# Performance work log

Hardware: AMD Instinct MI355X
Metric: run time of the kernel (lower is better)

The kernel has to match this reference:

```python
import jax, jax.numpy as jnp
import numpy as np

# Model config (matches init_kwargs)
HIDDEN = 2048
N_HEADS = 32
N_KV_HEADS = 8
HEAD_DIM = 64
BS = 8  # block_size_x = block_size_y = block_size_z


def setup_inputs() -> dict:
    key = jax.random.key(0)
    ks = jax.random.split(key, 5)
    B, X, Y, Z = 2, 16, 16, 16
    L = X * Y * Z  # 4096
    s = 1.0 / np.sqrt(HIDDEN)
    return {
        "hidden_states": jax.random.normal(ks[0], (B, L, HIDDEN), jnp.float32),
        "Wq": jax.random.normal(ks[1], (N_HEADS * HEAD_DIM, HIDDEN), jnp.float32) * s,
        "Wk": jax.random.normal(ks[2], (N_KV_HEADS * HEAD_DIM, HIDDEN), jnp.float32) * s,
        "Wv": jax.random.normal(ks[3], (N_KV_HEADS * HEAD_DIM, HIDDEN), jnp.float32) * s,
        "Wo": jax.random.normal(ks[4], (HIDDEN, N_HEADS * HEAD_DIM), jnp.float32) * s,
        "x_dim": 16,
        "y_dim": 16,
        "z_dim": 16,
    }


def _to_blocks(t, B, x_dim, y_dim, z_dim, H):
    # t: [B, L, H*D] with L interpreted as (x, y, z) row-major grid.
    # einops: 'b (bnx bsx bny bsy bnz bsz) (h d) -> (b bnx bny bnz) (bsx bsy bsz) h d'
    bnx, bny, bnz = x_dim // BS, y_dim // BS, z_dim // BS
    t = t.reshape(B, bnx, BS, bny, BS, bnz, BS, H, HEAD_DIM)
    t = t.transpose(0, 1, 3, 5, 2, 4, 6, 7, 8)  # [B,bnx,bny,bnz,bsx,bsy,bsz,H,D]
    return t.reshape(B * bnx * bny * bnz, BS * BS * BS, H, HEAD_DIM)


def _from_blocks(o, B, x_dim, y_dim, z_dim):
    bnx, bny, bnz = x_dim // BS, y_dim // BS, z_dim // BS
    o = o.reshape(B, bnx, bny, bnz, BS, BS, BS, N_HEADS, HEAD_DIM)
    o = o.transpose(0, 1, 4, 2, 5, 3, 6, 7, 8)  # back to (bnx bsx bny bsy bnz bsz)
    return o.reshape(B, x_dim * y_dim * z_dim, N_HEADS * HEAD_DIM)


def reference(hidden_states, Wq, Wk, Wv, Wo, x_dim, y_dim, z_dim):
    B, L, _ = hidden_states.shape
    q = _to_blocks(hidden_states @ Wq.T, B, x_dim, y_dim, z_dim, N_HEADS)     # [NB,T,H,D]
    k = _to_blocks(hidden_states @ Wk.T, B, x_dim, y_dim, z_dim, N_KV_HEADS)  # [NB,T,Hk,D]
    v = _to_blocks(hidden_states @ Wv.T, B, x_dim, y_dim, z_dim, N_KV_HEADS)
    # GQA: repeat kv heads across groups (flash_attn handles this internally)
    g = N_HEADS // N_KV_HEADS
    k = jnp.repeat(k, g, axis=2)
    v = jnp.repeat(v, g, axis=2)
    scale = HEAD_DIM ** -0.5
    # non-causal full attention within each 3D block
    scores = jnp.einsum('bthd,bshd->bhts', q, k) * scale  # [NB,H,T,T]
    p = jax.nn.softmax(scores, axis=-1)
    o = jnp.einsum('bhts,bshd->bthd', p, v)               # [NB,T,H,D]
    o = _from_blocks(o, B, x_dim, y_dim, z_dim)           # [B,L,H*D]
    return o @ Wo.T
```

## Files before the change

kernel.cpp:

```cpp
#include <hip/hip_runtime.h>

typedef _Float16 f16;
typedef _Float16 f16x4 __attribute__((ext_vector_type(4)));
typedef _Float16 f16x8 __attribute__((ext_vector_type(8)));
typedef float f32x4 __attribute__((ext_vector_type(4)));
typedef unsigned int u32;
typedef u32 u32x4 __attribute__((ext_vector_type(4)));

__device__ __forceinline__ f32x4 mfma16(f16x8 a, f16x8 b, f32x4 c) {
  return __builtin_amdgcn_mfma_f32_16x16x32_f16(a, b, c, 0, 0, 0);
}

__device__ __forceinline__ void gld_lds16(const void* g, void* l) {
  __builtin_amdgcn_global_load_lds(
      (const __attribute__((address_space(1))) void*)g,
      (__attribute__((address_space(3))) void*)l, 16, 0, 0);
}

__device__ __forceinline__ u32 pkrtz(float a, float b) {
  return __builtin_bit_cast(u32, __builtin_amdgcn_cvt_pkrtz(a, b));
}

#define XSWZ(row) (((row) & 7) << 4)

__global__ __launch_bounds__(256) void cast5_k(
    const float4* s0, const float4* s1, const float4* s2, const float4* s3,
    const float4* s4, f16x4* d0, f16x4* d1, f16x4* d2, f16x4* d3, f16x4* d4,
    int e0, int e1, int e2, int e3, int e4) {
  int i = blockIdx.x * blockDim.x + threadIdx.x;
  int stride = gridDim.x * blockDim.x;
  for (; i < e4; i += stride) {
    const float4* s = s0; f16x4* d = d0; int base = 0;
    if (i >= e0) { s = s1; d = d1; base = e0; }
    if (i >= e1) { s = s2; d = d2; base = e1; }
    if (i >= e2) { s = s3; d = d3; base = e2; }
    if (i >= e3) { s = s4; d = d4; base = e3; }
    float4 v = s[i - base];
    f16x4 o;
    o.x = (f16)v.x; o.y = (f16)v.y; o.z = (f16)v.z; o.w = (f16)v.w;
    d[i - base] = o;
  }
}

template <typename OutT>
__global__ __launch_bounds__(256, 2) void gemm_bt(
    const f16* __restrict__ A, const f16* __restrict__ B, OutT* __restrict__ C,
    int M, int N, int K, float oscale) {
  __shared__ __align__(16) f16 Al[128 * 64];
  __shared__ __align__(16) f16 Bl[128 * 64];
  const int tid = threadIdx.x;
  const int lane = tid & 63;
  const int wave = tid >> 6;
  const int bm = blockIdx.x, bn = blockIdx.y;
  const int wm = wave >> 1, wn = wave & 1;
  f32x4 acc[4][4] = {};

  const size_t ldb = (size_t)K * 2;
  const char* Ab = (const char*)A + (size_t)bm * 128 * ldb;
  const char* Bb = (const char*)B + (size_t)bn * 128 * ldb;

  const int kTiles = K >> 6;
  for (int kt = 0; kt < kTiles; ++kt) {
    const size_t kOff = (size_t)kt << 7;
    __syncthreads();
#pragma unroll
    for (int i = 0; i < 4; ++i) {
      int c = i * 256 + tid;
      int row = c >> 3;
      int colb = ((c & 7) << 4) ^ XSWZ(row);
      gld_lds16(Ab + (size_t)row * ldb + kOff + colb,
                (char*)Al + (i * 256 + wave * 64) * 16);
      gld_lds16(Bb + (size_t)row * ldb + kOff + colb,
                (char*)Bl + (i * 256 + wave * 64) * 16);
    }
    __syncthreads();
#pragma unroll
    for (int kk = 0; kk < 2; ++kk) {
      const int kb = kk * 64 + ((lane >> 4) << 4);
      f16x8 af[4], bf[4];
#pragma unroll
      for (int mf = 0; mf < 4; ++mf) {
        int row = wm * 64 + mf * 16 + (lane & 15);
        af[mf] = *(const f16x8*)((const char*)Al + (row << 7) + (kb ^ XSWZ(row)));
      }
#pragma unroll
      for (int nf = 0; nf < 4; ++nf) {
        int row = wn * 64 + nf * 16 + (lane & 15);
        bf[nf] = *(const f16x8*)((const char*)Bl + (row << 7) + (kb ^ XSWZ(row)));
      }
#pragma unroll
      for (int mf = 0; mf < 4; ++mf)
#pragma unroll
        for (int nf = 0; nf < 4; ++nf)
          acc[mf][nf] = mfma16(af[mf], bf[nf], acc[mf][nf]);
    }
  }
  const int r0 = ((lane >> 4) << 2);
  const int cl = lane & 15;
#pragma unroll
  for (int mf = 0; mf < 4; ++mf)
#pragma unroll
    for (int r = 0; r < 4; ++r) {
      size_t row = (size_t)bm * 128 + wm * 64 + mf * 16 + r0 + r;
#pragma unroll
      for (int nf = 0; nf < 4; ++nf) {
        int col = bn * 128 + wn * 64 + nf * 16 + cl;
        C[row * N + col] = (OutT)(acc[mf][nf][r] * oscale);
      }
    }
}

template <typename OutT>
__global__ __launch_bounds__(512, 2) void gemm_bt8(
    const f16* __restrict__ A, const f16* __restrict__ B, OutT* __restrict__ C,
    int M, int N, int K, float oscale) {
  __shared__ __align__(16) char lds[131072];
  const int tid = threadIdx.x;
  const int lane = tid & 63;
  const int wave = tid >> 6;
  const int wm = wave >> 2, wn = wave & 3;
  const int l15 = lane & 15, g = lane >> 4;
  const int bid = blockIdx.x;
  const int bm = (bid & 7) * 4 + ((bid >> 3) & 3);
  const int bn = bid >> 5;

  const size_t ldb = (size_t)K * 2;
  const int r0 = tid >> 2, r1 = 128 + (tid >> 2);
  const int chx = (((tid & 3) ^ ((tid >> 3) & 3)) << 4);
  const char* As0 = (const char*)A + (size_t)(bm * 256 + r0) * ldb + chx;
  const char* As1 = (const char*)A + (size_t)(bm * 256 + r1) * ldb + chx;
  const char* Bs0 = (const char*)B + (size_t)(bn * 256 + r0) * ldb + chx;
  const char* Bs1 = (const char*)B + (size_t)(bn * 256 + r1) * ldb + chx;

  auto stA = [&](int buf, int t, int kh) {
    char* dst = (char*)lds + (buf * 2 + kh) * 16384 + wave * 1024;
    size_t ko = (size_t)t * 128 + (size_t)kh * 64;
    gld_lds16(As0 + ko, dst);
    gld_lds16(As1 + ko, dst + 8192);
  };
  auto stB = [&](int buf, int t, int kh) {
    char* dst = (char*)lds + 65536 + (buf * 2 + kh) * 16384 + wave * 1024;
    size_t ko = (size_t)t * 128 + (size_t)kh * 64;
    gld_lds16(Bs0 + ko, dst);
    gld_lds16(Bs1 + ko, dst + 8192);
  };

  int aoff[8], boff[4];
  const int rsw = (g ^ ((l15 >> 1) & 3)) << 4;
#pragma unroll
  for (int mf = 0; mf < 8; ++mf)
    aoff[mf] = (wm * 128 + mf * 16 + l15) * 64 + rsw;
#pragma unroll
  for (int nf = 0; nf < 4; ++nf)
    boff[nf] = (wn * 64 + nf * 16 + l15) * 64 + rsw;

  f32x4 acc[8][4] = {};

  stA(0, 0, 0); stB(0, 0, 0); stA(0, 0, 1); stB(0, 0, 1);
  stA(1, 1, 0); stB(1, 1, 0); stA(1, 1, 1);
  asm volatile("s_waitcnt vmcnt(6)" ::: "memory");
  __builtin_amdgcn_s_barrier();

  const int nkt = K >> 6;
  for (int T = 0; T < nkt; ++T) {
    const int cur = T & 1;
    const char* A0 = (const char*)lds + (cur * 2 + 0) * 16384;
    const char* A1 = (const char*)lds + (cur * 2 + 1) * 16384;
    const char* B0r = (const char*)lds + 65536 + (cur * 2 + 0) * 16384;
    const char* B1r = (const char*)lds + 65536 + (cur * 2 + 1) * 16384;
    f16x8 a[8], b0, b1;
#pragma unroll
    for (int mf = 0; mf < 8; ++mf) a[mf] = *(const f16x8*)(A0 + aoff[mf]);
    b0 = *(const f16x8*)(B0r + boff[0]);
    b1 = *(const f16x8*)(B0r + boff[1]);
    if (T + 1 < nkt) stB(cur ^ 1, T + 1, 1);
    __builtin_amdgcn_s_barrier();
    __builtin_amdgcn_s_setprio(1);
#pragma unroll
    for (int mf = 0; mf < 8; ++mf) {
      acc[mf][0] = mfma16(a[mf], b0, acc[mf][0]);
      acc[mf][1] = mfma16(a[mf], b1, acc[mf][1]);
    }
    __builtin_amdgcn_s_setprio(0);
    __builtin_amdgcn_s_barrier();
    b0 = *(const f16x8*)(B0r + boff[2]);
    b1 = *(const f16x8*)(B0r + boff[3]);
    if (T + 2 < nkt) stA(cur, T + 2, 0);
    __builtin_amdgcn_s_barrier();
    __builtin_amdgcn_s_setprio(1);
#pragma unroll
    for (int mf = 0; mf < 8; ++mf) {
      acc[mf][2] = mfma16(a[mf], b0, acc[mf][2]);
      acc[mf][3] = mfma16(a[mf], b1, acc[mf][3]);
    }
    __builtin_amdgcn_s_setprio(0);
    __builtin_amdgcn_s_barrier();
#pragma unroll
    for (int mf = 0; mf < 8; ++mf) a[mf] = *(const f16x8*)(A1 + aoff[mf]);
    b0 = *(const f16x8*)(B1r + boff[0]);
    b1 = *(const f16x8*)(B1r + boff[1]);
    if (T + 2 < nkt) stB(cur, T + 2, 0);
    __builtin_amdgcn_s_barrier();
    __builtin_amdgcn_s_setprio(1);
#pragma unroll
    for (int mf = 0; mf < 8; ++mf) {
      acc[mf][0] = mfma16(a[mf], b0, acc[mf][0]);
      acc[mf][1] = mfma16(a[mf], b1, acc[mf][1]);
    }
    __builtin_amdgcn_s_setprio(0);
    __builtin_amdgcn_s_barrier();
    b0 = *(const f16x8*)(B1r + boff[2]);
    b1 = *(const f16x8*)(B1r + boff[3]);
    if (T + 2 < nkt) stA(cur, T + 2, 1);
    if (T < nkt - 2) asm volatile("s_waitcnt vmcnt(6)" ::: "memory");
    else             asm volatile("s_waitcnt vmcnt(0)" ::: "memory");
    __builtin_amdgcn_s_barrier();
    __builtin_amdgcn_s_setprio(1);
#pragma unroll
    for (int mf = 0; mf < 8; ++mf) {
      acc[mf][2] = mfma16(a[mf], b0, acc[mf][2]);
      acc[mf][3] = mfma16(a[mf], b1, acc[mf][3]);
    }
    __builtin_amdgcn_s_setprio(0);
    __builtin_amdgcn_s_barrier();
  }
#pragma unroll
  for (int mf = 0; mf < 8; ++mf)
#pragma unroll
    for (int r = 0; r < 4; ++r) {
      size_t row = (size_t)bm * 256 + wm * 128 + mf * 16 + g * 4 + r;
#pragma unroll
      for (int nf = 0; nf < 4; ++nf) {
        int col = bn * 256 + wn * 64 + nf * 16 + l15;
        C[row * (size_t)N + col] = (OutT)(acc[mf][nf][r] * oscale);
      }
    }
}

__device__ __forceinline__ int tok_row(int nb, int t) {
  int b = nb >> 3;
  int x = (((nb >> 2) & 1) << 3) | (t >> 6);
  int y = (((nb >> 1) & 1) << 3) | ((t >> 3) & 7);
  int z = ((nb & 1) << 3) | (t & 7);
  return (b << 12) | (x << 8) | (y << 4) | z;
}

__global__ __launch_bounds__(512) void attn3d(
    const f16* __restrict__ Q, const f16* __restrict__ KV, f16* __restrict__ O) {
  __shared__ __align__(16) f16 Ql[512 * 64];
  __shared__ __align__(16) f16 Kl[64 * 64];
  __shared__ __align__(16) f16 Vt[64 * 64];
  const int tid = threadIdx.x;
  const int lane = tid & 63;
  const int wave = tid >> 6;
  const int fid = blockIdx.x;
  const int orig = (fid & 7) * 64 + (fid >> 3);
  const int h = orig & 31, nb = orig >> 5;
  const int hk = h >> 2;
  const int l15 = lane & 15;
  const int g = lane >> 4;
  const size_t ldkv = 2048;

  const int pos2 = (((lane & 3) | (((lane >> 4) & 1) << 2) |
                     (((lane >> 2) & 3) << 3) | ((lane >> 5) << 5))) * 2;

#pragma unroll
  for (int i = 0; i < 8; ++i) {
    int c = i * 512 + tid;
    int row = c >> 3;
    int colb = ((c & 7) << 4) ^ XSWZ(row);
    gld_lds16((const char*)Q + (size_t)tok_row(nb, row) * 4096 + h * 128 + colb,
              (char*)Ql + (i * 512 + wave * 64) * 16);
  }
  __syncthreads();
  f16x8 bq[4][2];
#pragma unroll
  for (int qf = 0; qf < 4; ++qf)
#pragma unroll
    for (int kk = 0; kk < 2; ++kk) {
      int row = wave * 64 + qf * 16 + l15;
      int kb = kk * 64 + (g << 4);
      bq[qf][kk] = *(const f16x8*)((const char*)Ql + (row << 7) + (kb ^ XSWZ(row)));
    }

  f32x4 o[4][4] = {};
  float lacc[4] = {0.f, 0.f, 0.f, 0.f};

  for (int kt = 0; kt < 8; ++kt) {
    const int kv = tid & 63, dc = tid >> 6;
    f16x8 vch = *(const f16x8*)((const char*)KV +
        (size_t)tok_row(nb, kt * 64 + kv) * ldkv + 1024 + hk * 128 + dc * 16);
    __syncthreads();
    {
      int row = tid >> 3;
      int colb = ((tid & 7) << 4) ^ XSWZ(row);
      gld_lds16((const char*)KV + (size_t)tok_row(nb, kt * 64 + row) * ldkv + hk * 128 + colb,
                (char*)Kl + (wave * 64) * 16);
    }
    {
      const int dbase = wave * 8;
#pragma unroll
      for (int j = 0; j < 8; ++j)
        *(f16*)((char*)Vt + ((dbase + j) << 7) + (pos2 ^ (j << 4))) = vch[j];
    }
    __syncthreads();
    f32x4 s[4][4] = {};
    __builtin_amdgcn_s_setprio(1);
#pragma unroll
    for (int kk = 0; kk < 2; ++kk) {
      const int kb = kk * 64 + (g << 4);
      f16x8 ka[4];
#pragma unroll
      for (int nf = 0; nf < 4; ++nf) {
        int krow = nf * 16 + l15;
        ka[nf] = *(const f16x8*)((const char*)Kl + (krow << 7) + (kb ^ XSWZ(krow)));
      }
#pragma unroll
      for (int qf = 0; qf < 4; ++qf)
#pragma unroll
        for (int nf = 0; nf < 4; ++nf)
          s[qf][nf] = mfma16(ka[nf], bq[qf][kk], s[qf][nf]);
    }
    __builtin_amdgcn_s_setprio(0);
    u32x4 pf[4][2];
#pragma unroll
    for (int qf = 0; qf < 4; ++qf) {
      float ls = 0.f;
#pragma unroll
      for (int nf = 0; nf < 4; ++nf)
#pragma unroll
        for (int r = 0; r < 4; ++r) {
          float p = __builtin_amdgcn_exp2f(s[qf][nf][r]);
          s[qf][nf][r] = p;
          ls += p;
        }
      lacc[qf] += ls;
#pragma unroll
      for (int kh = 0; kh < 2; ++kh)
        pf[qf][kh] = u32x4{pkrtz(s[qf][2 * kh][0], s[qf][2 * kh][1]),
                           pkrtz(s[qf][2 * kh][2], s[qf][2 * kh][3]),
                           pkrtz(s[qf][2 * kh + 1][0], s[qf][2 * kh + 1][1]),
                           pkrtz(s[qf][2 * kh + 1][2], s[qf][2 * kh + 1][3])};
    }
    __builtin_amdgcn_s_setprio(1);
#pragma unroll
    for (int kh = 0; kh < 2; ++kh) {
      f16x8 va[4];
      const int cb = kh * 64 + g * 16;
#pragma unroll
      for (int df = 0; df < 4; ++df) {
        int d = df * 16 + l15;
        va[df] = *(const f16x8*)((const char*)Vt + (d << 7) + (cb ^ XSWZ(d)));
      }
#pragma unroll
      for (int qf = 0; qf < 4; ++qf) {
        f16x8 pfh = __builtin_bit_cast(f16x8, pf[qf][kh]);
#pragma unroll
        for (int df = 0; df < 4; ++df)
          o[qf][df] = mfma16(va[df], pfh, o[qf][df]);
      }
    }
    __builtin_amdgcn_s_setprio(0);
  }
#pragma unroll
  for (int qf = 0; qf < 4; ++qf) {
    float l = lacc[qf];
    l += __shfl_xor(l, 16);
    l += __shfl_xor(l, 32);
    float inv = 1.f / l;
    int t = wave * 64 + qf * 16 + l15;
    char* dst = (char*)O + (size_t)tok_row(nb, t) * 4096 + h * 128;
#pragma unroll
    for (int df = 0; df < 4; ++df) {
      f16x4 o4;
#pragma unroll
      for (int r = 0; r < 4; ++r) o4[r] = (f16)(o[qf][df][r] * inv);
      *(f16x4*)(dst + df * 32 + g * 8) = o4;
    }
  }
}

extern "C" void kernel_launch(void* const* d_in, const int* in_sizes, int n_in,
                              void* d_out, int out_size, void* d_ws, size_t ws_size,
                              hipStream_t stream) {
  (void)in_sizes; (void)n_in; (void)out_size; (void)ws_size;
  const float* hs = (const float*)d_in[0];
  const float* Wq = (const float*)d_in[1];
  const float* Wk = (const float*)d_in[2];
  const float* Wv = (const float*)d_in[3];
  const float* Wo = (const float*)d_in[4];
  float* out = (float*)d_out;
  char* ws = (char*)d_ws;

  f16* hid16 = (f16*)(ws + 0);
  f16* Wq16  = (f16*)(ws + 33554432);
  f16* Wk16  = (f16*)(ws + 41943040);
  f16* Wv16  = (f16*)(ws + 44040192);
  f16* Wo16  = (f16*)(ws + 46137344);
  f16* Q16   = (f16*)(ws + 54525952);
  f16* KV16  = (f16*)(ws + 88080384);

  cast5_k<<<2048, 256, 0, stream>>>(
      (const float4*)hs, (const float4*)Wq, (const float4*)Wk,
      (const float4*)Wv, (const float4*)Wo,
      (f16x4*)hid16, (f16x4*)Wq16, (f16x4*)Wk16, (f16x4*)Wv16, (f16x4*)Wo16,
      4194304, 5242880, 5505024, 5767168, 6815744);

  gemm_bt8<f16><<<256, 512, 0, stream>>>(hid16, Wq16, Q16, 8192, 2048, 2048,
                                         0.18033688011112042f);
  gemm_bt<f16><<<dim3(64, 8), 256, 0, stream>>>(hid16, Wk16, KV16, 8192, 1024, 2048, 1.0f);

  attn3d<<<512, 512, 0, stream>>>(Q16, KV16, hid16);

  gemm_bt8<float><<<256, 512, 0, stream>>>(hid16, Wo16, out, 8192, 2048, 2048, 1.0f);
}
```

Before: 269.4 us.

## Double-buffer K/V tiles in attention and load Q directly into registers

The attention kernel now keeps two LDS buffers for K and transposed V. It prefetches the next KV tile while computing the current one, which cuts the per-iteration barriers from two to one. Q is read straight from global memory into registers instead of being staged through a 64KB LDS buffer. This frees LDS, which may allow more resident blocks. Packing P to f16 is moved inline next to the PV MFMAs. The costs are extra live registers for the prefetched V chunk and less coalesced direct Q loads.

New measurement: 268.2 us. Within noise of the previous version (-0.5%).

```diff
diff --git a/kernel.cpp b/kernel.cpp
--- a/kernel.cpp
+++ b/kernel.cpp
@@ -247,9 +247,8 @@
 
 __global__ __launch_bounds__(512) void attn3d(
     const f16* __restrict__ Q, const f16* __restrict__ KV, f16* __restrict__ O) {
-  __shared__ __align__(16) f16 Ql[512 * 64];
-  __shared__ __align__(16) f16 Kl[64 * 64];
-  __shared__ __align__(16) f16 Vt[64 * 64];
+  __shared__ __align__(16) f16 Kl[2][64 * 64];
+  __shared__ __align__(16) f16 Vt[2][64 * 64];
   const int tid = threadIdx.x;
   const int lane = tid & 63;
   const int wave = tid >> 6;
@@ -264,46 +263,46 @@
   const int pos2 = (((lane & 3) | (((lane >> 4) & 1) << 2) |
                      (((lane >> 2) & 3) << 3) | ((lane >> 5) << 5))) * 2;
 
-#pragma unroll
-  for (int i = 0; i < 8; ++i) {
-    int c = i * 512 + tid;
-    int row = c >> 3;
-    int colb = ((c & 7) << 4) ^ XSWZ(row);
-    gld_lds16((const char*)Q + (size_t)tok_row(nb, row) * 4096 + h * 128 + colb,
-              (char*)Ql + (i * 512 + wave * 64) * 16);
-  }
-  __syncthreads();
+  const int krow = tid >> 3;
+  const int kcolb = ((tid & 7) << 4) ^ XSWZ(krow);
+
   f16x8 bq[4][2];
 #pragma unroll
-  for (int qf = 0; qf < 4; ++qf)
-#pragma unroll
-    for (int kk = 0; kk < 2; ++kk) {
-      int row = wave * 64 + qf * 16 + l15;
-      int kb = kk * 64 + (g << 4);
-      bq[qf][kk] = *(const f16x8*)((const char*)Ql + (row << 7) + (kb ^ XSWZ(row)));
-    }
+  for (int qf = 0; qf < 4; ++qf) {
+    const char* qrow = (const char*)Q +
+        (size_t)tok_row(nb, wave * 64 + qf * 16 + l15) * 4096 + h * 128;
+#pragma unroll
+    for (int kk = 0; kk < 2; ++kk)
+      bq[qf][kk] = *(const f16x8*)(qrow + kk * 64 + g * 16);
+  }
+
+  {
+    gld_lds16((const char*)KV + (size_t)tok_row(nb, krow) * ldkv + hk * 128 + kcolb,
+              (char*)Kl[0] + wave * 1024);
+    f16x8 vch = *(const f16x8*)((const char*)KV +
+        (size_t)tok_row(nb, lane) * ldkv + 1024 + hk * 128 + wave * 16);
+    asm volatile("s_waitcnt vmcnt(0)" ::: "memory");
+    const int dbase = wave * 8;
+#pragma unroll
+    for (int j = 0; j < 8; ++j)
+      *(f16*)((char*)Vt[0] + ((dbase + j) << 7) + (pos2 ^ (j << 4))) = vch[j];
+    __syncthreads();
+  }
 
   f32x4 o[4][4] = {};
   float lacc[4] = {0.f, 0.f, 0.f, 0.f};
 
   for (int kt = 0; kt < 8; ++kt) {
-    const int kv = tid & 63, dc = tid >> 6;
-    f16x8 vch = *(const f16x8*)((const char*)KV +
-        (size_t)tok_row(nb, kt * 64 + kv) * ldkv + 1024 + hk * 128 + dc * 16);
-    __syncthreads();
-    {
-      int row = tid >> 3;
-      int colb = ((tid & 7) << 4) ^ XSWZ(row);
-      gld_lds16((const char*)KV + (size_t)tok_row(nb, kt * 64 + row) * ldkv + hk * 128 + colb,
-                (char*)Kl + (wave * 64) * 16);
-    }
-    {
-      const int dbase = wave * 8;
-#pragma unroll
-      for (int j = 0; j < 8; ++j)
-        *(f16*)((char*)Vt + ((dbase + j) << 7) + (pos2 ^ (j << 4))) = vch[j];
-    }
-    __syncthreads();
+    const int b = kt & 1;
+    const char* Kb = (const char*)Kl[b];
+    const char* Vb = (const char*)Vt[b];
+    f16x8 vch;
+    if (kt < 7) {
+      gld_lds16((const char*)KV + (size_t)tok_row(nb, (kt + 1) * 64 + krow) * ldkv + hk * 128 + kcolb,
+                (char*)Kl[b ^ 1] + wave * 1024);
+      vch = *(const f16x8*)((const char*)KV +
+          (size_t)tok_row(nb, (kt + 1) * 64 + lane) * ldkv + 1024 + hk * 128 + wave * 16);
+    }
     f32x4 s[4][4] = {};
     __builtin_amdgcn_s_setprio(1);
 #pragma unroll
@@ -312,8 +311,8 @@
       f16x8 ka[4];
 #pragma unroll
       for (int nf = 0; nf < 4; ++nf) {
-        int krow = nf * 16 + l15;
-        ka[nf] = *(const f16x8*)((const char*)Kl + (krow << 7) + (kb ^ XSWZ(krow)));
+        int kr = nf * 16 + l15;
+        ka[nf] = *(const f16x8*)(Kb + (kr << 7) + (kb ^ XSWZ(kr)));
       }
 #pragma unroll
       for (int qf = 0; qf < 4; ++qf)
@@ -322,7 +321,6 @@
           s[qf][nf] = mfma16(ka[nf], bq[qf][kk], s[qf][nf]);
     }
     __builtin_amdgcn_s_setprio(0);
-    u32x4 pf[4][2];
 #pragma unroll
     for (int qf = 0; qf < 4; ++qf) {
       float ls = 0.f;
@@ -335,12 +333,6 @@
           ls += p;
         }
       lacc[qf] += ls;
-#pragma unroll
-      for (int kh = 0; kh < 2; ++kh)
-        pf[qf][kh] = u32x4{pkrtz(s[qf][2 * kh][0], s[qf][2 * kh][1]),
-                           pkrtz(s[qf][2 * kh][2], s[qf][2 * kh][3]),
-                           pkrtz(s[qf][2 * kh + 1][0], s[qf][2 * kh + 1][1]),
-                           pkrtz(s[qf][2 * kh + 1][2], s[qf][2 * kh + 1][3])};
     }
     __builtin_amdgcn_s_setprio(1);
 #pragma unroll
@@ -350,17 +342,29 @@
 #pragma unroll
       for (int df = 0; df < 4; ++df) {
         int d = df * 16 + l15;
-        va[df] = *(const f16x8*)((const char*)Vt + (d << 7) + (cb ^ XSWZ(d)));
+        va[df] = *(const f16x8*)(Vb + (d << 7) + (cb ^ XSWZ(d)));
       }
 #pragma unroll
       for (int qf = 0; qf < 4; ++qf) {
-        f16x8 pfh = __builtin_bit_cast(f16x8, pf[qf][kh]);
+        u32x4 pw = {pkrtz(s[qf][2 * kh][0], s[qf][2 * kh][1]),
+                    pkrtz(s[qf][2 * kh][2], s[qf][2 * kh][3]),
+                    pkrtz(s[qf][2 * kh + 1][0], s[qf][2 * kh + 1][1]),
+                    pkrtz(s[qf][2 * kh + 1][2], s[qf][2 * kh + 1][3])};
+        f16x8 pfh = __builtin_bit_cast(f16x8, pw);
 #pragma unroll
         for (int df = 0; df < 4; ++df)
           o[qf][df] = mfma16(va[df], pfh, o[qf][df]);
       }
     }
     __builtin_amdgcn_s_setprio(0);
+    if (kt < 7) {
+      asm volatile("s_waitcnt vmcnt(0)" ::: "memory");
+      const int dbase = wave * 8;
+#pragma unroll
+      for (int j = 0; j < 8; ++j)
+        *(f16*)((char*)Vt[b ^ 1] + ((dbase + j) << 7) + (pos2 ^ (j << 4))) = vch[j];
+      __syncthreads();
+    }
   }
 #pragma unroll
   for (int qf = 0; qf < 4; ++qf) {
```
